# Performance work log

Measured on AMD Instinct MI355X. Metric: run time of the kernel, lower is better.

The kernel has to match this reference:

```python
import jax, jax.numpy as jnp
import numpy as np

B, L, D, H = 2, 2048, 1024, 16
HD = D // H

def setup_inputs() -> dict:
    key = jax.random.key(0)
    ks = jax.random.split(key, 9)
    s = 1.0 / np.sqrt(D)
    return {
        "x": jax.random.normal(ks[0], (B, L, D), jnp.float32),
        "Wq": jax.random.normal(ks[1], (D, D), jnp.float32) * s,
        "bq": jax.random.normal(ks[2], (D,), jnp.float32) * 0.02,
        "Wk": jax.random.normal(ks[3], (D, D), jnp.float32) * s,
        "bk": jax.random.normal(ks[4], (D,), jnp.float32) * 0.02,
        "Wv": jax.random.normal(ks[5], (D, D), jnp.float32) * s,
        "bv": jax.random.normal(ks[6], (D,), jnp.float32) * 0.02,
        "Wo": jax.random.normal(ks[7], (D, D), jnp.float32) * s,
        "bo": jax.random.normal(ks[8], (D,), jnp.float32) * 0.02,
    }

def reference(x, Wq, bq, Wk, bk, Wv, bv, Wo, bo):
    b, l, d = x.shape
    # projections -> [B, H, L, HD]
    def split_heads(t):
        return t.reshape(b, l, H, HD).transpose(0, 2, 1, 3)
    Q = split_heads(x @ Wq + bq)
    K = split_heads(x @ Wk + bk)
    V = split_heads(x @ Wv + bv)
    scores = jnp.einsum('bhqd,bhkd->bhqk', Q, K)  # [B,H,L,L]
    causal = jnp.tril(jnp.ones((l, l), bool))
    scores = jnp.where(causal, scores, -jnp.inf)
    attn = jax.nn.softmax(scores / np.sqrt(HD), axis=-1)
    ctx = jnp.einsum('bhqk,bhkd->bhqd', attn, V)
    ctx = ctx.transpose(0, 2, 1, 3).reshape(b, l, d)
    return ctx @ Wo + bo
```

## Files before the change

### kernel.cpp

```cpp
#include <hip/hip_runtime.h>
#include <stdint.h>

typedef unsigned short u16;
typedef __attribute__((ext_vector_type(8))) __bf16 bf16x8;
typedef __attribute__((ext_vector_type(4))) float f32x4;
typedef __attribute__((ext_vector_type(16))) float f32x16;

__device__ __forceinline__ u16 f2bf(float f) {
  union { float f; uint32_t u; } c; c.f = f;
  uint32_t u = c.u + 0x7fffu + ((c.u >> 16) & 1u);
  return (u16)(u >> 16);
}
__device__ __forceinline__ uint32_t cvtpk(float a, float b) {
  uint32_t r;
  asm("v_cvt_pk_bf16_f32 %0, %1, %2" : "=v"(r) : "v"(a), "v"(b));
  return r;
}

__device__ __forceinline__ void async16(const u16* g, u16* l) {
  __builtin_amdgcn_global_load_lds(
      (const __attribute__((address_space(1))) void*)g,
      (__attribute__((address_space(3))) void*)l, 16, 0, 0);
}

__device__ __forceinline__ f32x4 mfma16(bf16x8 a, bf16x8 b, f32x4 c) {
  return __builtin_amdgcn_mfma_f32_16x16x32_bf16(a, b, c, 0, 0, 0);
}
__device__ __forceinline__ f32x16 mfma32(bf16x8 a, bf16x8 b, f32x16 c) {
  return __builtin_amdgcn_mfma_f32_32x32x16_bf16(a, b, c, 0, 0, 0);
}


__global__ __launch_bounds__(256) void x_cvt_kernel(const float* __restrict__ x,
                                                    u16* __restrict__ xb) {
  int i = (blockIdx.x * 256 + threadIdx.x) * 4;
  float4 v = *(const float4*)(x + i);
  uint2 t; t.x = cvtpk(v.x, v.y); t.y = cvtpk(v.z, v.w);
  *(uint2*)(xb + i) = t;
}

__global__ __launch_bounds__(256) void wt_cvt_kernel(const float* __restrict__ Wq,
                                                     const float* __restrict__ Wk,
                                                     const float* __restrict__ Wv,
                                                     const float* __restrict__ Wo,
                                                     u16* __restrict__ out) {
  __shared__ __align__(16) u16 t[64][72];
  int z = blockIdx.z;
  const float* W = (z == 0) ? Wq : (z == 1) ? Wk : (z == 2) ? Wv : Wo;
  u16* o = out + (size_t)z * (1u << 20);
  int n0 = blockIdx.x * 64, k0 = blockIdx.y * 64;
  int tid = threadIdx.x;
  int c4 = (tid & 15) * 4, r0 = tid >> 4;
#pragma unroll
  for (int i = 0; i < 4; i++) {
    int r = r0 + i * 16;
    float4 v = *(const float4*)(W + (size_t)(k0 + r) * 1024 + n0 + c4);
    t[c4 + 0][r] = f2bf(v.x);
    t[c4 + 1][r] = f2bf(v.y);
    t[c4 + 2][r] = f2bf(v.z);
    t[c4 + 3][r] = f2bf(v.w);
  }
  __syncthreads();
  int n = tid >> 2, kc = (tid & 3) * 16;
  uint4 a = *(const uint4*)&t[n][kc];
  uint4 b = *(const uint4*)&t[n][kc + 8];
  *(uint4*)(o + (size_t)(n0 + n) * 1024 + k0 + kc) = a;
  *(uint4*)(o + (size_t)(n0 + n) * 1024 + k0 + kc + 8) = b;
}

template <int TN>
__device__ __forceinline__ void gemm_core3(const u16* __restrict__ A,
                                           const u16* __restrict__ Bt,
                                           u16* As, u16* Bs,
                                           f32x4 (&acc)[4][TN / 32],
                                           int m0, int n0) {
  constexpr int NJ = TN / 32;
  constexpr int ASZ = 128 * 32, BSZ = TN * 32;
  const int tid = threadIdx.x, wave = tid >> 6, lane = tid & 63;
  const int low = lane & 15, hi = lane >> 4;
  const int wm = wave >> 1, wn = wave & 1;
  const f32x4 fzero = {0.f, 0.f, 0.f, 0.f};
#pragma unroll
  for (int i = 0; i < 4; i++)
#pragma unroll
    for (int j = 0; j < NJ; j++) acc[i][j] = fzero;

  const int ea0 = wave * 128 + lane, ea1 = ea0 + 64;
  const u16* ga0 = A + (size_t)(m0 + (ea0 >> 2)) * 1024 + (ea0 & 3) * 8;
  const u16* ga1 = A + (size_t)(m0 + (ea1 >> 2)) * 1024 + (ea1 & 3) * 8;
  u16* la0 = As + (wave * 2 + 0) * 512;
  u16* la1 = As + (wave * 2 + 1) * 512;

  const int eb0 = (TN == 128) ? (wave * 128 + lane) : (wave * 64 + lane);
  const int eb1 = eb0 + 64;
  const u16* gb0 = Bt + (size_t)(n0 + (eb0 >> 2)) * 1024 + (eb0 & 3) * 8;
  const u16* gb1 = Bt + (size_t)(n0 + (eb1 >> 2)) * 1024 + (eb1 & 3) * 8;
  u16* lb0 = Bs + ((TN == 128) ? (wave * 2 + 0) * 512 : wave * 512);
  u16* lb1 = Bs + (wave * 2 + 1) * 512;

  const u16* ap = As + (wm * 64 + low) * 32 + hi * 8;
  const u16* bp = Bs + (wn * (TN / 2) + low) * 32 + hi * 8;

#define GSTAGE(buf, KT)                                                        \
  {                                                                            \
    async16(ga0 + (KT), la0 + (buf) * ASZ);                                    \
    async16(ga1 + (KT), la1 + (buf) * ASZ);                                    \
    async16(gb0 + (KT), lb0 + (buf) * BSZ);                                    \
    if (TN == 128) async16(gb1 + (KT), lb1 + (buf) * BSZ);                     \
  }

  GSTAGE(0, 0)
  GSTAGE(1, 32)
  GSTAGE(2, 64)
  int buf = 0;
  for (int kt = 0; kt < 1024; kt += 32) {
    if (kt + 96 <= 1024) {
      if constexpr (TN == 128) asm volatile("s_waitcnt vmcnt(8)" ::: "memory");
      else                     asm volatile("s_waitcnt vmcnt(6)" ::: "memory");
    } else if (kt + 64 <= 1024) {
      if constexpr (TN == 128) asm volatile("s_waitcnt vmcnt(4)" ::: "memory");
      else                     asm volatile("s_waitcnt vmcnt(3)" ::: "memory");
    } else {
      asm volatile("s_waitcnt vmcnt(0)" ::: "memory");
    }
    __builtin_amdgcn_s_barrier();

    bf16x8 af[4], bfv[NJ];
#pragma unroll
    for (int i = 0; i < 4; i++)
      af[i] = *(const bf16x8*)(ap + buf * ASZ + i * 16 * 32);
#pragma unroll
    for (int j = 0; j < NJ; j++)
      bfv[j] = *(const bf16x8*)(bp + buf * BSZ + j * 16 * 32);
#pragma unroll
    for (int i = 0; i < 4; i++)
#pragma unroll
      for (int j = 0; j < NJ; j++) acc[i][j] = mfma16(af[i], bfv[j], acc[i][j]);

    __builtin_amdgcn_s_barrier();
    if (kt + 96 < 1024) GSTAGE(buf, kt + 96)
    buf = (buf == 2) ? 0 : buf + 1;
  }
#undef GSTAGE
}

__global__ __launch_bounds__(256) void gemm_qkv_kernel(
    const u16* __restrict__ xb, const u16* __restrict__ wT,
    const float* __restrict__ bq, const float* __restrict__ bk,
    const float* __restrict__ bv,
    u16* __restrict__ qs, u16* __restrict__ ks, u16* __restrict__ vts) {
  __shared__ __align__(16) u16 smem[24576];
  u16* As = smem;
  u16* Bs = smem + 12288;

  const int bid = blockIdx.x;
  const int c = bid & 7;
  const int j = bid >> 3;
  const int z = j >> 5;
  const int jj = j & 31;
  const int ytile = (c >> 1) * 8 + (jj >> 2);
  const int xtile = (c & 1) * 4 + (jj & 3);
  const int m0 = ytile * 128, n0 = xtile * 128;

  const u16* Bt = wT + (size_t)z * (1u << 20);
  f32x4 acc[4][4];
  gemm_core3<128>(xb, Bt, As, Bs, acc, m0, n0);

  const float* bias = (z == 0) ? bq : (z == 1) ? bk : bv;
  u16* out = (z == 0) ? qs : (z == 1) ? ks : vts;
  const float scale = (z == 0) ? 0.180336880f : 1.0f;
  const int tid = threadIdx.x, wave = tid >> 6, lane = tid & 63;
  const int low = lane & 15, hi = lane >> 4;
  const int wm = wave >> 1, wn = wave & 1;

  const int h = (n0 >> 6) + wn;
  const int gmb = m0 + wm * 64;
  const int b = gmb >> 11;
  const int lb = gmb & 2047;

  u16* tile = smem + wave * 4360;
#pragma unroll
  for (int i = 0; i < 4; i++)
#pragma unroll
    for (int jx = 0; jx < 4; jx++) {
      int hd = jx * 16 + low;
      float bval = bias[h * 64 + hd];
#pragma unroll
      for (int r = 0; r < 4; r++) {
        int row = i * 16 + hi * 4 + r;
        tile[row * 68 + hd] = f2bf((acc[i][jx][r] + bval) * scale);
      }
    }

  if (z != 2) {
    u16* dst = out + ((size_t)((b * 16 + h) * 2048 + lb + lane)) * 64;
    const u16* src = tile + lane * 68;
#pragma unroll
    for (int cc = 0; cc < 4; cc++) {
      uint2 a0 = *(const uint2*)(src + cc * 16 + 0);
      uint2 a1 = *(const uint2*)(src + cc * 16 + 4);
      uint2 a2 = *(const uint2*)(src + cc * 16 + 8);
      uint2 a3 = *(const uint2*)(src + cc * 16 + 12);
      uint4 w0; w0.x = a0.x; w0.y = a0.y; w0.z = a1.x; w0.w = a1.y;
      uint4 w1; w1.x = a2.x; w1.y = a2.y; w1.z = a3.x; w1.w = a3.y;
      *(uint4*)(dst + cc * 16 + 0) = w0;
      *(uint4*)(dst + cc * 16 + 8) = w1;
    }
  } else {
    int l4 = (lane & 15) * 4;
    int lp4 = (l4 & ~12) | ((l4 & 4) << 1) | ((l4 & 8) >> 1);
    int ghd = lane >> 4;
    u16* vbase = out + ((size_t)(b * 16 + h) * 64) * 2048 + lb + lp4;
#pragma unroll
    for (int s = 0; s < 16; s++) {
      int hd = s * 4 + ghd;
      uint32_t v0 = tile[(l4 + 0) * 68 + hd];
      uint32_t v1 = tile[(l4 + 1) * 68 + hd];
      uint32_t v2 = tile[(l4 + 2) * 68 + hd];
      uint32_t v3 = tile[(l4 + 3) * 68 + hd];
      uint2 w; w.x = v0 | (v1 << 16); w.y = v2 | (v3 << 16);
      *(uint2*)(vbase + (size_t)hd * 2048) = w;
    }
  }
}

__global__ __launch_bounds__(256) void gemm_out_kernel(
    const u16* __restrict__ ctx, const u16* __restrict__ woT,
    const float* __restrict__ bo, float* __restrict__ out) {
  __shared__ __align__(16) u16 As[3 * 128 * 32];
  __shared__ __align__(16) u16 Bs[3 * 64 * 32];

  const int bid = blockIdx.x;
  const int c = bid & 7;
  const int j = bid >> 3;
  const int ytile = (c >> 1) * 8 + (j >> 3);
  const int xtile = (c & 1) * 8 + (j & 7);
  const int m0 = ytile * 128, n0 = xtile * 64;

  f32x4 acc[4][2];
  gemm_core3<64>(ctx, woT, As, Bs, acc, m0, n0);
  const int tid = threadIdx.x, wave = tid >> 6, lane = tid & 63;
  const int low = lane & 15, hi = lane >> 4;
  const int wm = wave >> 1, wn = wave & 1;
#pragma unroll
  for (int i = 0; i < 4; i++)
#pragma unroll
    for (int jx = 0; jx < 2; jx++) {
      int gn = n0 + wn * 32 + jx * 16 + low;
      float bval = bo[gn];
#pragma unroll
      for (int r = 0; r < 4; r++) {
        int gm = m0 + wm * 64 + i * 16 + hi * 4 + r;
        out[(size_t)gm * 1024 + gn] = acc[i][jx][r] + bval;
      }
    }
}

__global__ __launch_bounds__(512) void flash_kernel(
    const u16* __restrict__ Qs, const u16* __restrict__ Ks,
    const u16* __restrict__ Vts, u16* __restrict__ ctx) {
  __shared__ __align__(16) u16 Kls[2][2][64 * 64];
  __shared__ __align__(16) u16 Vls[2][2][64 * 64];

  const int bid = blockIdx.x;
  const int qt = (bid < 256) ? (15 - (bid >> 5)) : ((bid - 256) >> 5);
  const int bh = bid & 31;
  const int qb = qt * 128;
  const int nT = qt + 1;

  const int tid = threadIdx.x, wave = tid >> 6, lane = tid & 63;
  const int wq = wave & 3, g = wave >> 2;
  const int q32 = lane & 31, hi2 = lane >> 5;
  const int x7 = q32 & 7;

  const u16* Qb = Qs + (size_t)bh * (2048 * 64);
  const u16* Kb = Ks + (size_t)bh * (2048 * 64);
  const u16* Vb = Vts + (size_t)bh * (64 * 2048);

  const int qrow = qb + wq * 32 + q32;
  bf16x8 qf[4];
#pragma unroll
  for (int ds = 0; ds < 4; ds++)
    qf[ds] = *(const bf16x8*)(Qb + (size_t)qrow * 64 + ds * 16 + hi2 * 8);

  f32x16 o0, o1;
#pragma unroll
  for (int r = 0; r < 16; r++) { o0[r] = 0.f; o1[r] = 0.f; }
  float m_ = -1e30f, l_ = 0.f;

#define STAGE(buf, KT0)                                                        \
  {                                                                            \
    _Pragma("unroll") for (int i = 0; i < 2; i++) {                            \
      int row = (wq * 2 + i) * 8 + (lane >> 3);                                \
      async16(Kb + (size_t)((KT0) + row) * 64 +                                \
                  (((lane & 7) ^ (row & 7)) * 8),                              \
              &Kls[g][buf][(wq * 2 + i) * 512]);                               \
      async16(Vb + (size_t)row * 2048 + (KT0) +                                \
                  (((lane & 7) ^ (row & 7)) * 8),                              \
              &Vls[g][buf][(wq * 2 + i) * 512]);                               \
    }                                                                          \
  }

  const int tb = g * nT;
  STAGE(0, (tb + 0) * 64)
  STAGE(1, (tb + 1) * 64)

  const int qmax = qb + wq * 32 + 31;

  int cur = 0;
  for (int t = 0; t < nT; t++) {
    const int kt0 = (tb + t) * 64;
    if (t + 1 < nT) { asm volatile("s_waitcnt vmcnt(4)" ::: "memory"); }
    else            { asm volatile("s_waitcnt vmcnt(0)" ::: "memory"); }
    __builtin_amdgcn_s_barrier();

    if (kt0 <= qmax) {
      const u16* Kc = &Kls[g][cur][0];
      const u16* Vc = &Vls[g][cur][0];

      f32x16 s0, s1;
#pragma unroll
      for (int r = 0; r < 16; r++) { s0[r] = 0.f; s1[r] = 0.f; }
      __builtin_amdgcn_s_setprio(1);
#pragma unroll
      for (int ds = 0; ds < 4; ds++) {
        int cs = ((ds * 2 + hi2) ^ x7) * 8;
        bf16x8 kf0 = *(const bf16x8*)(Kc + q32 * 64 + cs);
        bf16x8 kf1 = *(const bf16x8*)(Kc + (32 + q32) * 64 + cs);
        s0 = mfma32(kf0, qf[ds], s0);
        s1 = mfma32(kf1, qf[ds], s1);
      }
      __builtin_amdgcn_s_setprio(0);

      bf16x8 vf0[4], vf1[4];
#pragma unroll
      for (int ksx = 0; ksx < 4; ksx++) {
        int sc = ((2 * ksx + hi2) ^ x7) * 8;
        vf0[ksx] = *(const bf16x8*)(Vc + q32 * 64 + sc);
        vf1[ksx] = *(const bf16x8*)(Vc + (32 + q32) * 64 + sc);
      }

      if (kt0 + 63 > qb + wq * 32) {
#pragma unroll
        for (int r = 0; r < 16; r++) {
          int kl = (r & 3) + 8 * (r >> 2) + 4 * hi2;
          if (kt0 + kl > qrow) s0[r] = -1e30f;
          if (kt0 + 32 + kl > qrow) s1[r] = -1e30f;
        }
      }

      float pm = -1e30f;
#pragma unroll
      for (int r = 0; r < 16; r++) pm = fmaxf(pm, fmaxf(s0[r], s1[r]));
      pm = fmaxf(pm, __shfl_xor(pm, 32));
      if (__any(pm > m_ + 8.f)) {
        float mn = fmaxf(m_, pm);
        float corr = __builtin_amdgcn_exp2f(m_ - mn);
        m_ = mn;
        l_ *= corr;
#pragma unroll
        for (int r = 0; r < 16; r++) { o0[r] *= corr; o1[r] *= corr; }
      }

      float rs = 0.f;
#pragma unroll
      for (int r = 0; r < 16; r++) {
        s0[r] = __builtin_amdgcn_exp2f(s0[r] - m_);
        s1[r] = __builtin_amdgcn_exp2f(s1[r] - m_);
        rs += s0[r] + s1[r];
      }
      rs += __shfl_xor(rs, 32);
      l_ += rs;

      bf16x8 pb[4];
#pragma unroll
      for (int ksx = 0; ksx < 4; ksx++) {
        union { uint32_t u[4]; bf16x8 v; } pu;
        if (ksx < 2) {
          int rb = 8 * ksx;
          pu.u[0] = cvtpk(s0[rb + 0], s0[rb + 1]);
          pu.u[1] = cvtpk(s0[rb + 2], s0[rb + 3]);
          pu.u[2] = cvtpk(s0[rb + 4], s0[rb + 5]);
          pu.u[3] = cvtpk(s0[rb + 6], s0[rb + 7]);
        } else {
          int rb = 8 * (ksx - 2);
          pu.u[0] = cvtpk(s1[rb + 0], s1[rb + 1]);
          pu.u[1] = cvtpk(s1[rb + 2], s1[rb + 3]);
          pu.u[2] = cvtpk(s1[rb + 4], s1[rb + 5]);
          pu.u[3] = cvtpk(s1[rb + 6], s1[rb + 7]);
        }
        pb[ksx] = pu.v;
      }

      __builtin_amdgcn_s_setprio(1);
#pragma unroll
      for (int ksx = 0; ksx < 4; ksx++) {
        o0 = mfma32(vf0[ksx], pb[ksx], o0);
        o1 = mfma32(vf1[ksx], pb[ksx], o1);
      }
      __builtin_amdgcn_s_setprio(0);
    }

    __builtin_amdgcn_s_barrier();
    if (t + 2 < nT) STAGE(cur, (tb + t + 2) * 64)
    cur ^= 1;
  }

  __syncthreads();
  float* mb = (float*)&Kls[0][0][0] + wq * 2304;
  if (g == 1) {
#pragma unroll
    for (int m = 0; m < 4; m++) {
      f32x4 qa = {o0[4 * m + 0], o0[4 * m + 1], o0[4 * m + 2], o0[4 * m + 3]};
      f32x4 qb2 = {o1[4 * m + 0], o1[4 * m + 1], o1[4 * m + 2], o1[4 * m + 3]};
      *(f32x4*)(mb + m * 256 + (lane << 2)) = qa;
      *(f32x4*)(mb + (4 + m) * 256 + (lane << 2)) = qb2;
    }
    mb[2048 + (lane << 1) + 0] = m_;
    mb[2048 + (lane << 1) + 1] = l_;
  }
  __syncthreads();
  if (g == 0) {
    float m1 = mb[2048 + (lane << 1) + 0];
    float l1 = mb[2048 + (lane << 1) + 1];
    float mm = fmaxf(m_, m1);
    float cA = __builtin_amdgcn_exp2f(m_ - mm);
    float cB = __builtin_amdgcn_exp2f(m1 - mm);
    l_ = l_ * cA + l1 * cB;
#pragma unroll
    for (int m = 0; m < 4; m++) {
      f32x4 qa = *(const f32x4*)(mb + m * 256 + (lane << 2));
      f32x4 qb2 = *(const f32x4*)(mb + (4 + m) * 256 + (lane << 2));
#pragma unroll
      for (int jx = 0; jx < 4; jx++) {
        o0[4 * m + jx] = o0[4 * m + jx] * cA + qa[jx] * cB;
        o1[4 * m + jx] = o1[4 * m + jx] * cA + qb2[jx] * cB;
      }
    }

    const int b = bh >> 4, h = bh & 15;
    float inv = 1.f / l_;
    size_t base = ((size_t)(b * 2048 + qrow)) * 1024 + h * 64;
#pragma unroll
    for (int m = 0; m < 4; m++) {
      uint2 w0, w1;
      w0.x = cvtpk(o0[4 * m + 0] * inv, o0[4 * m + 1] * inv);
      w0.y = cvtpk(o0[4 * m + 2] * inv, o0[4 * m + 3] * inv);
      *(uint2*)(ctx + base + 8 * m + 4 * hi2) = w0;
      w1.x = cvtpk(o1[4 * m + 0] * inv, o1[4 * m + 1] * inv);
      w1.y = cvtpk(o1[4 * m + 2] * inv, o1[4 * m + 3] * inv);
      *(uint2*)(ctx + base + 32 + 8 * m + 4 * hi2) = w1;
    }
  }
}


extern "C" void kernel_launch(void* const* d_in, const int* in_sizes, int n_in,
                              void* d_out, int out_size, void* d_ws, size_t ws_size,
                              hipStream_t stream) {
  const float* x  = (const float*)d_in[0];
  const float* Wq = (const float*)d_in[1];
  const float* bq = (const float*)d_in[2];
  const float* Wk = (const float*)d_in[3];
  const float* bk = (const float*)d_in[4];
  const float* Wv = (const float*)d_in[5];
  const float* bv = (const float*)d_in[6];
  const float* Wo = (const float*)d_in[7];
  const float* bo = (const float*)d_in[8];

  char* ws = (char*)d_ws;
  u16* xb  = (u16*)(ws);
  u16* wT  = (u16*)(ws + (8u << 20));
  u16* qs  = (u16*)(ws + (16u << 20));
  u16* ks  = (u16*)(ws + (24u << 20));
  u16* vts = (u16*)(ws + (32u << 20));
  u16* ctx = (u16*)(ws + (40u << 20));

  x_cvt_kernel<<<4096, 256, 0, stream>>>(x, xb);
  wt_cvt_kernel<<<dim3(16, 16, 4), 256, 0, stream>>>(Wq, Wk, Wv, Wo, wT);
  gemm_qkv_kernel<<<768, 256, 0, stream>>>(xb, wT, bq, bk, bv, qs, ks, vts);
  flash_kernel<<<512, 512, 0, stream>>>(qs, ks, vts, ctx);
  gemm_out_kernel<<<512, 256, 0, stream>>>(ctx, wT + 3 * (1u << 20), bo, (float*)d_out);
}
```

Baseline: 114.5 us.

## Split KV range of long causal query tiles across two blocks with merge kernel

Query tiles in the upper half of the sequence now have their key/value range split into two segments, each handled by its own block. Each segment writes unnormalized-then-normalized partial outputs plus row max and sum to scratch space reused from the already consumed x and weight buffers. A new merge kernel combines the two partials into the context tensor. The aim is to even out per-block work under causal masking and raise the block count for better CU utilization. The cost is an extra kernel launch, extra global traffic for the partials, and bf16 rounding of the intermediate outputs.

```diff
diff --git a/kernel.cpp b/kernel.cpp
--- a/kernel.cpp
+++ b/kernel.cpp
@@ -10,6 +10,9 @@
   union { float f; uint32_t u; } c; c.f = f;
   uint32_t u = c.u + 0x7fffu + ((c.u >> 16) & 1u);
   return (u16)(u >> 16);
+}
+__device__ __forceinline__ float bf2f(u16 v) {
+  union { uint32_t u; float f; } c; c.u = ((uint32_t)v) << 16; return c.f;
 }
 __device__ __forceinline__ uint32_t cvtpk(float a, float b) {
   uint32_t r;
@@ -258,15 +261,32 @@
 
 __global__ __launch_bounds__(512) void flash_kernel(
     const u16* __restrict__ Qs, const u16* __restrict__ Ks,
-    const u16* __restrict__ Vts, u16* __restrict__ ctx) {
+    const u16* __restrict__ Vts, u16* __restrict__ ctx,
+    u16* __restrict__ pO, float* __restrict__ pML) {
   __shared__ __align__(16) u16 Kls[2][2][64 * 64];
   __shared__ __align__(16) u16 Vls[2][2][64 * 64];
 
   const int bid = blockIdx.x;
-  const int qt = (bid < 256) ? (15 - (bid >> 5)) : ((bid - 256) >> 5);
-  const int bh = bid & 31;
+  int qt, bh, seg, nseg;
+  if (bid < 512) {
+    qt = 15 - (bid >> 6);
+    seg = (bid & 63) >> 5;
+    bh = bid & 31;
+    nseg = 2;
+  } else {
+    qt = 7 - ((bid - 512) >> 5);
+    bh = (bid - 512) & 31;
+    seg = 0;
+    nseg = 1;
+  }
   const int qb = qt * 128;
-  const int nT = qt + 1;
+  const int nkv = 2 * qt + 2;
+  const int len0 = (qt + 2) & ~1;
+  int wstart, wlen;
+  if (nseg == 1) { wstart = 0; wlen = nkv; }
+  else if (seg == 0) { wstart = 0; wlen = len0; }
+  else { wstart = len0; wlen = nkv - len0; }
+  const int nT = wlen >> 1;
 
   const int tid = threadIdx.x, wave = tid >> 6, lane = tid & 63;
   const int wq = wave & 3, g = wave >> 2;
@@ -301,7 +321,7 @@
     }                                                                          \
   }
 
-  const int tb = g * nT;
+  const int tb = wstart + g * nT;
   STAGE(0, (tb + 0) * 64)
   STAGE(1, (tb + 1) * 64)
 
@@ -426,6 +446,7 @@
     float mm = fmaxf(m_, m1);
     float cA = __builtin_amdgcn_exp2f(m_ - mm);
     float cB = __builtin_amdgcn_exp2f(m1 - mm);
+    m_ = mm;
     l_ = l_ * cA + l1 * cB;
 #pragma unroll
     for (int m = 0; m < 4; m++) {
@@ -438,19 +459,83 @@
       }
     }
 
-    const int b = bh >> 4, h = bh & 15;
-    float inv = 1.f / l_;
-    size_t base = ((size_t)(b * 2048 + qrow)) * 1024 + h * 64;
-#pragma unroll
-    for (int m = 0; m < 4; m++) {
-      uint2 w0, w1;
-      w0.x = cvtpk(o0[4 * m + 0] * inv, o0[4 * m + 1] * inv);
-      w0.y = cvtpk(o0[4 * m + 2] * inv, o0[4 * m + 3] * inv);
-      *(uint2*)(ctx + base + 8 * m + 4 * hi2) = w0;
-      w1.x = cvtpk(o1[4 * m + 0] * inv, o1[4 * m + 1] * inv);
-      w1.y = cvtpk(o1[4 * m + 2] * inv, o1[4 * m + 3] * inv);
-      *(uint2*)(ctx + base + 32 + 8 * m + 4 * hi2) = w1;
-    }
+    float inv = (l_ > 0.f) ? 1.f / l_ : 0.f;
+    if (nseg == 1) {
+      const int b = bh >> 4, h = bh & 15;
+      size_t base = ((size_t)(b * 2048 + qrow)) * 1024 + h * 64;
+#pragma unroll
+      for (int m = 0; m < 4; m++) {
+        uint2 w0, w1;
+        w0.x = cvtpk(o0[4 * m + 0] * inv, o0[4 * m + 1] * inv);
+        w0.y = cvtpk(o0[4 * m + 2] * inv, o0[4 * m + 3] * inv);
+        *(uint2*)(ctx + base + 8 * m + 4 * hi2) = w0;
+        w1.x = cvtpk(o1[4 * m + 0] * inv, o1[4 * m + 1] * inv);
+        w1.y = cvtpk(o1[4 * m + 2] * inv, o1[4 * m + 3] * inv);
+        *(uint2*)(ctx + base + 32 + 8 * m + 4 * hi2) = w1;
+      }
+    } else {
+      const int sidx = (qt - 8) * 64 + seg * 32 + bh;
+      const int lr = wq * 32 + q32;
+      u16* base = pO + (size_t)sidx * 8192 + lr * 64;
+#pragma unroll
+      for (int m = 0; m < 4; m++) {
+        uint2 w0, w1;
+        w0.x = cvtpk(o0[4 * m + 0] * inv, o0[4 * m + 1] * inv);
+        w0.y = cvtpk(o0[4 * m + 2] * inv, o0[4 * m + 3] * inv);
+        *(uint2*)(base + 8 * m + 4 * hi2) = w0;
+        w1.x = cvtpk(o1[4 * m + 0] * inv, o1[4 * m + 1] * inv);
+        w1.y = cvtpk(o1[4 * m + 2] * inv, o1[4 * m + 3] * inv);
+        *(uint2*)(base + 32 + 8 * m + 4 * hi2) = w1;
+      }
+      if (hi2 == 0) {
+        pML[(size_t)sidx * 256 + lr * 2 + 0] = m_;
+        pML[(size_t)sidx * 256 + lr * 2 + 1] = l_;
+      }
+    }
+  }
+}
+
+__global__ __launch_bounds__(256) void flash_merge_kernel(
+    const u16* __restrict__ pO, const float* __restrict__ pML,
+    u16* __restrict__ ctx) {
+  const int u = blockIdx.x;
+  const int qt = 8 + (u >> 5);
+  const int bh = u & 31;
+  const int s0 = (qt - 8) * 64 + bh;
+  const int s1 = s0 + 32;
+  const int tid = threadIdx.x;
+  const int row = tid >> 1;
+  const int dh = (tid & 1) * 32;
+
+  float m0 = pML[(size_t)s0 * 256 + row * 2 + 0];
+  float l0 = pML[(size_t)s0 * 256 + row * 2 + 1];
+  float m1 = pML[(size_t)s1 * 256 + row * 2 + 0];
+  float l1 = pML[(size_t)s1 * 256 + row * 2 + 1];
+  float mm = fmaxf(m0, m1);
+  float w0 = l0 * __builtin_amdgcn_exp2f(m0 - mm);
+  float w1 = l1 * __builtin_amdgcn_exp2f(m1 - mm);
+  float inv = 1.f / (w0 + w1);
+  w0 *= inv; w1 *= inv;
+
+  const u16* a = pO + (size_t)s0 * 8192 + row * 64 + dh;
+  const u16* b = pO + (size_t)s1 * 8192 + row * 64 + dh;
+  const int bb = bh >> 4, h = bh & 15;
+  const int qrow = qt * 128 + row;
+  u16* dst = ctx + ((size_t)(bb * 2048 + qrow)) * 1024 + h * 64 + dh;
+
+#pragma unroll
+  for (int i = 0; i < 32; i += 8) {
+    union { uint4 u4; u16 s[8]; } ua, ub;
+    ua.u4 = *(const uint4*)(a + i);
+    ub.u4 = *(const uint4*)(b + i);
+    float f[8];
+#pragma unroll
+    for (int k = 0; k < 8; k++)
+      f[k] = bf2f(ua.s[k]) * w0 + bf2f(ub.s[k]) * w1;
+    uint4 o4;
+    o4.x = cvtpk(f[0], f[1]); o4.y = cvtpk(f[2], f[3]);
+    o4.z = cvtpk(f[4], f[5]); o4.w = cvtpk(f[6], f[7]);
+    *(uint4*)(dst + i) = o4;
   }
 }
 
@@ -476,9 +561,13 @@
   u16* vts = (u16*)(ws + (32u << 20));
   u16* ctx = (u16*)(ws + (40u << 20));
 
+  u16* pO = xb;
+  float* pML = (float*)wT;
+
   x_cvt_kernel<<<4096, 256, 0, stream>>>(x, xb);
   wt_cvt_kernel<<<dim3(16, 16, 4), 256, 0, stream>>>(Wq, Wk, Wv, Wo, wT);
   gemm_qkv_kernel<<<768, 256, 0, stream>>>(xb, wT, bq, bk, bv, qs, ks, vts);
-  flash_kernel<<<512, 512, 0, stream>>>(qs, ks, vts, ctx);
+  flash_kernel<<<768, 512, 0, stream>>>(qs, ks, vts, ctx, pO, pML);
+  flash_merge_kernel<<<256, 256, 0, stream>>>(pO, pML, ctx);
   gemm_out_kernel<<<512, 256, 0, stream>>>(ctx, wT + 3 * (1u << 20), bo, (float*)d_out);
 }
```

Result: no change. 116.2 us (+1.5%).

## Load V fragments directly from global, drop V LDS staging, pack merge in bf16

Applied to the files above, without the earlier changes.

V tiles are no longer staged through LDS with async copies. Each lane now reads its V fragments straight from global memory at the top of each tile, which halves the LDS footprint and the async-load traffic, and the wait count drops from 4 to 2 to match. The cross-half shuffle for the row max now runs only when a rescale is needed. The final merge of the two key-split wave groups passes partial outputs through LDS as packed bf16 instead of fp32, which cuts shared-memory traffic but loses precision in the merged accumulator. Direct global V loads may add latency that is no longer hidden by the double-buffered prefetch.

```diff
diff --git a/kernel.cpp b/kernel.cpp
--- a/kernel.cpp
+++ b/kernel.cpp
@@ -10,6 +10,9 @@
   union { float f; uint32_t u; } c; c.f = f;
   uint32_t u = c.u + 0x7fffu + ((c.u >> 16) & 1u);
   return (u16)(u >> 16);
+}
+__device__ __forceinline__ float bf2f(uint32_t v) {
+  union { uint32_t u; float f; } c; c.u = v << 16; return c.f;
 }
 __device__ __forceinline__ uint32_t cvtpk(float a, float b) {
   uint32_t r;
@@ -260,7 +263,6 @@
     const u16* __restrict__ Qs, const u16* __restrict__ Ks,
     const u16* __restrict__ Vts, u16* __restrict__ ctx) {
   __shared__ __align__(16) u16 Kls[2][2][64 * 64];
-  __shared__ __align__(16) u16 Vls[2][2][64 * 64];
 
   const int bid = blockIdx.x;
   const int qt = (bid < 256) ? (15 - (bid >> 5)) : ((bid - 256) >> 5);
@@ -295,9 +297,6 @@
       async16(Kb + (size_t)((KT0) + row) * 64 +                                \
                   (((lane & 7) ^ (row & 7)) * 8),                              \
               &Kls[g][buf][(wq * 2 + i) * 512]);                               \
-      async16(Vb + (size_t)row * 2048 + (KT0) +                                \
-                  (((lane & 7) ^ (row & 7)) * 8),                              \
-              &Vls[g][buf][(wq * 2 + i) * 512]);                               \
     }                                                                          \
   }
 
@@ -306,17 +305,26 @@
   STAGE(1, (tb + 1) * 64)
 
   const int qmax = qb + wq * 32 + 31;
+  const u16* vG0 = Vb + (size_t)q32 * 2048;
+  const u16* vG1 = Vb + (size_t)(32 + q32) * 2048;
 
   int cur = 0;
   for (int t = 0; t < nT; t++) {
     const int kt0 = (tb + t) * 64;
-    if (t + 1 < nT) { asm volatile("s_waitcnt vmcnt(4)" ::: "memory"); }
+    if (t + 1 < nT) { asm volatile("s_waitcnt vmcnt(2)" ::: "memory"); }
     else            { asm volatile("s_waitcnt vmcnt(0)" ::: "memory"); }
     __builtin_amdgcn_s_barrier();
 
     if (kt0 <= qmax) {
       const u16* Kc = &Kls[g][cur][0];
-      const u16* Vc = &Vls[g][cur][0];
+
+      bf16x8 vf0[4], vf1[4];
+#pragma unroll
+      for (int ksx = 0; ksx < 4; ksx++) {
+        int sc = (2 * ksx + hi2) * 8;
+        vf0[ksx] = *(const bf16x8*)(vG0 + kt0 + sc);
+        vf1[ksx] = *(const bf16x8*)(vG1 + kt0 + sc);
+      }
 
       f32x16 s0, s1;
 #pragma unroll
@@ -332,14 +340,6 @@
       }
       __builtin_amdgcn_s_setprio(0);
 
-      bf16x8 vf0[4], vf1[4];
-#pragma unroll
-      for (int ksx = 0; ksx < 4; ksx++) {
-        int sc = ((2 * ksx + hi2) ^ x7) * 8;
-        vf0[ksx] = *(const bf16x8*)(Vc + q32 * 64 + sc);
-        vf1[ksx] = *(const bf16x8*)(Vc + (32 + q32) * 64 + sc);
-      }
-
       if (kt0 + 63 > qb + wq * 32) {
 #pragma unroll
         for (int r = 0; r < 16; r++) {
@@ -349,11 +349,11 @@
         }
       }
 
-      float pm = -1e30f;
-#pragma unroll
-      for (int r = 0; r < 16; r++) pm = fmaxf(pm, fmaxf(s0[r], s1[r]));
-      pm = fmaxf(pm, __shfl_xor(pm, 32));
-      if (__any(pm > m_ + 8.f)) {
+      float lpm = -1e30f;
+#pragma unroll
+      for (int r = 0; r < 16; r++) lpm = fmaxf(lpm, fmaxf(s0[r], s1[r]));
+      if (__any(lpm > m_ + 8.f)) {
+        float pm = fmaxf(lpm, __shfl_xor(lpm, 32));
         float mn = fmaxf(m_, pm);
         float corr = __builtin_amdgcn_exp2f(m_ - mn);
         m_ = mn;
@@ -407,35 +407,40 @@
   }
 
   __syncthreads();
-  float* mb = (float*)&Kls[0][0][0] + wq * 2304;
+  uint32_t* sc32 = (uint32_t*)&Kls[0][0][0];
+  uint32_t* mb = sc32 + wq * 1152 + lane * 16;
+  float* mlf = (float*)(sc32 + wq * 1152 + 1024);
   if (g == 1) {
 #pragma unroll
     for (int m = 0; m < 4; m++) {
-      f32x4 qa = {o0[4 * m + 0], o0[4 * m + 1], o0[4 * m + 2], o0[4 * m + 3]};
-      f32x4 qb2 = {o1[4 * m + 0], o1[4 * m + 1], o1[4 * m + 2], o1[4 * m + 3]};
-      *(f32x4*)(mb + m * 256 + (lane << 2)) = qa;
-      *(f32x4*)(mb + (4 + m) * 256 + (lane << 2)) = qb2;
-    }
-    mb[2048 + (lane << 1) + 0] = m_;
-    mb[2048 + (lane << 1) + 1] = l_;
+      mb[2 * m + 0] = cvtpk(o0[4 * m + 0], o0[4 * m + 1]);
+      mb[2 * m + 1] = cvtpk(o0[4 * m + 2], o0[4 * m + 3]);
+      mb[8 + 2 * m + 0] = cvtpk(o1[4 * m + 0], o1[4 * m + 1]);
+      mb[8 + 2 * m + 1] = cvtpk(o1[4 * m + 2], o1[4 * m + 3]);
+    }
+    mlf[(lane << 1) + 0] = m_;
+    mlf[(lane << 1) + 1] = l_;
   }
   __syncthreads();
   if (g == 0) {
-    float m1 = mb[2048 + (lane << 1) + 0];
-    float l1 = mb[2048 + (lane << 1) + 1];
+    float m1 = mlf[(lane << 1) + 0];
+    float l1 = mlf[(lane << 1) + 1];
     float mm = fmaxf(m_, m1);
     float cA = __builtin_amdgcn_exp2f(m_ - mm);
     float cB = __builtin_amdgcn_exp2f(m1 - mm);
     l_ = l_ * cA + l1 * cB;
 #pragma unroll
     for (int m = 0; m < 4; m++) {
-      f32x4 qa = *(const f32x4*)(mb + m * 256 + (lane << 2));
-      f32x4 qb2 = *(const f32x4*)(mb + (4 + m) * 256 + (lane << 2));
-#pragma unroll
-      for (int jx = 0; jx < 4; jx++) {
-        o0[4 * m + jx] = o0[4 * m + jx] * cA + qa[jx] * cB;
-        o1[4 * m + jx] = o1[4 * m + jx] * cA + qb2[jx] * cB;
-      }
+      uint32_t pa0 = mb[2 * m + 0], pa1 = mb[2 * m + 1];
+      uint32_t pb0 = mb[8 + 2 * m + 0], pb1 = mb[8 + 2 * m + 1];
+      o0[4 * m + 0] = o0[4 * m + 0] * cA + bf2f(pa0 & 0xffffu) * cB;
+      o0[4 * m + 1] = o0[4 * m + 1] * cA + bf2f(pa0 >> 16) * cB;
+      o0[4 * m + 2] = o0[4 * m + 2] * cA + bf2f(pa1 & 0xffffu) * cB;
+      o0[4 * m + 3] = o0[4 * m + 3] * cA + bf2f(pa1 >> 16) * cB;
+      o1[4 * m + 0] = o1[4 * m + 0] * cA + bf2f(pb0 & 0xffffu) * cB;
+      o1[4 * m + 1] = o1[4 * m + 1] * cA + bf2f(pb0 >> 16) * cB;
+      o1[4 * m + 2] = o1[4 * m + 2] * cA + bf2f(pb1 & 0xffffu) * cB;
+      o1[4 * m + 3] = o1[4 * m + 3] * cA + bf2f(pb1 >> 16) * cB;
     }
 
     const int b = bh >> 4, h = bh & 15;
```

Measured after the change: 142.4 us. +24.4%, slower.

## Single-buffer V tiles in LDS and defer cross-half max shuffle in flash kernel

Applied to the files above, without the earlier changes.

K stays double-buffered two tiles ahead, but V now uses a single buffer loaded one tile ahead. This cuts the flash kernel's LDS footprint from 64KB to 48KB, which may allow more resident blocks per CU, at the cost of a shorter prefetch distance for V. The wait count drops to match the fewer outstanding loads. The row-max shuffle across lane halves now runs only inside the rescale branch, after a lane-local threshold test, removing a shuffle from the common path.

```diff
diff --git a/kernel.cpp b/kernel.cpp
--- a/kernel.cpp
+++ b/kernel.cpp
@@ -259,8 +259,7 @@
 __global__ __launch_bounds__(512) void flash_kernel(
     const u16* __restrict__ Qs, const u16* __restrict__ Ks,
     const u16* __restrict__ Vts, u16* __restrict__ ctx) {
-  __shared__ __align__(16) u16 Kls[2][2][64 * 64];
-  __shared__ __align__(16) u16 Vls[2][2][64 * 64];
+  __shared__ __align__(16) u16 smem[24576];
 
   const int bid = blockIdx.x;
   const int qt = (bid < 256) ? (15 - (bid >> 5)) : ((bid - 256) >> 5);
@@ -277,6 +276,9 @@
   const u16* Kb = Ks + (size_t)bh * (2048 * 64);
   const u16* Vb = Vts + (size_t)bh * (64 * 2048);
 
+  u16* Kg = smem + g * 8192;
+  u16* Vg = smem + 16384 + g * 4096;
+
   const int qrow = qb + wq * 32 + q32;
   bf16x8 qf[4];
 #pragma unroll
@@ -288,35 +290,42 @@
   for (int r = 0; r < 16; r++) { o0[r] = 0.f; o1[r] = 0.f; }
   float m_ = -1e30f, l_ = 0.f;
 
-#define STAGE(buf, KT0)                                                        \
+#define STAGE_K(buf, KT0)                                                      \
   {                                                                            \
     _Pragma("unroll") for (int i = 0; i < 2; i++) {                            \
       int row = (wq * 2 + i) * 8 + (lane >> 3);                                \
       async16(Kb + (size_t)((KT0) + row) * 64 +                                \
                   (((lane & 7) ^ (row & 7)) * 8),                              \
-              &Kls[g][buf][(wq * 2 + i) * 512]);                               \
+              Kg + (buf) * 4096 + (wq * 2 + i) * 512);                         \
+    }                                                                          \
+  }
+#define STAGE_V(KT0)                                                           \
+  {                                                                            \
+    _Pragma("unroll") for (int i = 0; i < 2; i++) {                            \
+      int row = (wq * 2 + i) * 8 + (lane >> 3);                                \
       async16(Vb + (size_t)row * 2048 + (KT0) +                                \
                   (((lane & 7) ^ (row & 7)) * 8),                              \
-              &Vls[g][buf][(wq * 2 + i) * 512]);                               \
+              Vg + (wq * 2 + i) * 512);                                        \
     }                                                                          \
   }
 
   const int tb = g * nT;
-  STAGE(0, (tb + 0) * 64)
-  STAGE(1, (tb + 1) * 64)
+  STAGE_V(tb * 64)
+  STAGE_K(0, (tb + 0) * 64)
+  STAGE_K(1, (tb + 1) * 64)
 
   const int qmax = qb + wq * 32 + 31;
 
   int cur = 0;
   for (int t = 0; t < nT; t++) {
     const int kt0 = (tb + t) * 64;
-    if (t + 1 < nT) { asm volatile("s_waitcnt vmcnt(4)" ::: "memory"); }
+    if (t + 1 < nT) { asm volatile("s_waitcnt vmcnt(2)" ::: "memory"); }
     else            { asm volatile("s_waitcnt vmcnt(0)" ::: "memory"); }
     __builtin_amdgcn_s_barrier();
 
     if (kt0 <= qmax) {
-      const u16* Kc = &Kls[g][cur][0];
-      const u16* Vc = &Vls[g][cur][0];
+      const u16* Kc = Kg + cur * 4096;
+      const u16* Vc = Vg;
 
       f32x16 s0, s1;
 #pragma unroll
@@ -349,11 +358,11 @@
         }
       }
 
-      float pm = -1e30f;
-#pragma unroll
-      for (int r = 0; r < 16; r++) pm = fmaxf(pm, fmaxf(s0[r], s1[r]));
-      pm = fmaxf(pm, __shfl_xor(pm, 32));
-      if (__any(pm > m_ + 8.f)) {
+      float lpm = -1e30f;
+#pragma unroll
+      for (int r = 0; r < 16; r++) lpm = fmaxf(lpm, fmaxf(s0[r], s1[r]));
+      if (__any(lpm > m_ + 8.f)) {
+        float pm = fmaxf(lpm, __shfl_xor(lpm, 32));
         float mn = fmaxf(m_, pm);
         float corr = __builtin_amdgcn_exp2f(m_ - mn);
         m_ = mn;
@@ -402,12 +411,13 @@
     }
 
     __builtin_amdgcn_s_barrier();
-    if (t + 2 < nT) STAGE(cur, (tb + t + 2) * 64)
+    if (t + 1 < nT) STAGE_V((tb + t + 1) * 64)
+    if (t + 2 < nT) STAGE_K(cur, (tb + t + 2) * 64)
     cur ^= 1;
   }
 
   __syncthreads();
-  float* mb = (float*)&Kls[0][0][0] + wq * 2304;
+  float* mb = (float*)smem + wq * 2304;
   if (g == 1) {
 #pragma unroll
     for (int m = 0; m < 4; m++) {
```

Result: slower. 118.0 us (+3.0%).
